# Optimization experiments

Measured on AMD Instinct MI355X. Metric: run time of the kernel, lower is better.

Reference implementation:

```python
import jax, jax.numpy as jnp
import numpy as np

# column-index constants for the node feature matrix and edge attributes
VM, VA, PG, QG, PD, QD = 0, 1, 2, 3, 4, 5
G_COL, B_COL = 0, 1

N_NODES = 100000
N_EDGES = 3200000
N_FEAT = 6


def setup_inputs() -> dict:
    key = jax.random.key(0)
    k1, k2, k3, k4, k5, k6 = jax.random.split(key, 6)
    pred = jax.random.normal(k1, (N_NODES, N_FEAT), dtype=jnp.float32)
    target = jax.random.normal(k2, (N_NODES, N_FEAT), dtype=jnp.float32)
    src = jax.random.randint(k3, (N_EDGES,), 0, N_NODES, dtype=jnp.int32)
    dst = jax.random.randint(k4, (N_EDGES,), 0, N_NODES, dtype=jnp.int32)
    edge_index = jnp.stack([src, dst], axis=0)
    edge_attr = jax.random.normal(k5, (N_EDGES, 2), dtype=jnp.float32)
    mask = jax.random.bernoulli(k6, 0.5, (N_NODES, N_FEAT))
    return {"pred": pred, "target": target, "edge_index": edge_index,
            "edge_attr": edge_attr, "mask": mask}


def reference(pred, target, edge_index, edge_attr, mask):
    # temp_pred[~mask] = target[~mask]
    tp = jnp.where(mask, pred, target)

    V_m = tp[:, VM]
    V_a = tp[:, VA]
    V = V_m * jnp.exp(1j * V_a)           # complex64 [N]
    V_conj = jnp.conj(V)

    # conj(Y_bus) entries on edges: G - jB
    Y_conj = edge_attr[:, G_COL] - 1j * edge_attr[:, B_COL]  # complex64 [E]

    row, col = edge_index[0], edge_index[1]
    # (Y_bus_conj @ V_conj)[i] = sum over edges (i,j) of conj(Y_ij) * conj(V_j)
    msg = Y_conj * V_conj[col]                               # gather-multiply [E]
    matvec = jax.ops.segment_sum(msg, row, num_segments=tp.shape[0])  # scatter-add [N]

    S_injection = V * matvec                                  # diag(V) @ (...)

    net_P = tp[:, PG] - tp[:, PD]
    net_Q = tp[:, QG] - tp[:, QD]
    diff = (net_P + 1j * net_Q) - S_injection

    loss = jnp.mean(jnp.abs(diff))
    real_loss = jnp.mean(jnp.abs(jnp.real(diff)))
    imag_loss = jnp.mean(jnp.abs(jnp.imag(diff)))
    return (loss, real_loss, imag_loss)
```

## Files before the change

kernel.cpp:

```cpp
#include <hip/hip_runtime.h>
#include <math.h>

constexpr int N_NODES = 100000;
constexpr int N_EDGES = 3200000;
constexpr int NF      = 6;

constexpr int BSHIFT  = 10;
constexpr int BNODES  = 1 << BSHIFT;
constexpr int NB      = (N_NODES + BNODES - 1) >> BSHIFT;
constexpr int CAP     = 34816;
constexpr int NSLICE  = 8;
constexpr int TILE    = 2048;
constexpr int EPT     = TILE / 256;
constexpr int NBLK_PART = (N_EDGES + TILE - 1) / TILE;

constexpr size_t OFF_V    = 0;
constexpr size_t OFF_MSG  = OFF_V + (size_t)N_NODES * 8;
constexpr size_t OFF_LROW = OFF_MSG + (size_t)NB * CAP * 8;
constexpr size_t OFF_PART = OFF_LROW + (size_t)NB * CAP * 2;
constexpr size_t OFF_CNT  = OFF_PART + (size_t)NB * NSLICE * BNODES * 8;
constexpr int    CTR_WORDS = 1024 / 4;
constexpr size_t WS_NEED  = OFF_CNT + 1024;

union F2U { float2 f; unsigned long long u; };

__global__ void node_prep(const float* __restrict__ pred,
                          const float* __restrict__ target,
                          const unsigned char* __restrict__ mask,
                          float2* __restrict__ v,
                          unsigned int* __restrict__ ctr) {
    int i = blockIdx.x * blockDim.x + threadIdx.x;
    if (blockIdx.x == 0 && threadIdx.x < CTR_WORDS) ctr[threadIdx.x] = 0u;
    if (i >= N_NODES) return;
    const int b = i * NF;
    float vm = mask[b + 0] ? pred[b + 0] : target[b + 0];
    float va = mask[b + 1] ? pred[b + 1] : target[b + 1];
    float s, c;
    sincosf(va, &s, &c);
    v[i] = make_float2(vm * c, vm * s);
}

__global__ __launch_bounds__(256) void partition_edges(
        const int* __restrict__ row, const int* __restrict__ col,
        const float2* __restrict__ attr, const float2* __restrict__ v,
        unsigned int* __restrict__ gcur,
        unsigned short* __restrict__ lrow_g, float2* __restrict__ msg_g) {
    __shared__ unsigned int h[4][NB];
    __shared__ unsigned int cur[4][NB];
    __shared__ int wb[4][NB];
    __shared__ int dbase[NB];
    __shared__ unsigned int tot_s[NB];
    __shared__ unsigned int rr_s[TILE];
    __shared__ float2 msg_s[TILE];
    __shared__ int total_s;

    const int tid = threadIdx.x;
    const int w = tid >> 6;
    const int e0 = blockIdx.x * TILE;

    for (int i = tid; i < 4 * NB; i += 256) {
        (&h[0][0])[i] = 0u;
        (&cur[0][0])[i] = 0u;
    }
    __syncthreads();

    int r[EPT];
    #pragma unroll
    for (int k = 0; k < EPT; ++k) {
        int e = e0 + k * 256 + tid;
        if (e < N_EDGES) {
            r[k] = row[e];
            atomicAdd(&h[w][r[k] >> BSHIFT], 1u);
        } else {
            r[k] = -1;
        }
    }
    __syncthreads();

    if (tid < NB)
        tot_s[tid] = h[0][tid] + h[1][tid] + h[2][tid] + h[3][tid];
    __syncthreads();

    if (tid < NB) {
        int lbase = 0;
        for (int j = 0; j < tid; ++j) lbase += (int)tot_s[j];
        unsigned t0 = h[0][tid], t1 = h[1][tid], t2 = h[2][tid];
        unsigned tot = tot_s[tid];
        unsigned g = tot ? atomicAdd(&gcur[tid], tot) : 0u;
        dbase[tid] = (int)g - lbase;
        wb[0][tid] = lbase;
        wb[1][tid] = lbase + (int)t0;
        wb[2][tid] = lbase + (int)(t0 + t1);
        wb[3][tid] = lbase + (int)(t0 + t1 + t2);
        if (tid == NB - 1) total_s = lbase + (int)tot;
    }
    __syncthreads();

    #pragma unroll
    for (int k = 0; k < EPT; ++k) {
        int rr = r[k];
        if (rr < 0) continue;
        int e = e0 + k * 256 + tid;
        int b = rr >> BSHIFT;
        int slot = wb[w][b] + (int)atomicAdd(&cur[w][b], 1u);
        int c = col[e];
        float2 gb = attr[e];
        float2 vv = v[c];
        float mre = fmaf(gb.x, vv.x, -gb.y * vv.y);
        float mim = -fmaf(gb.x, vv.y, gb.y * vv.x);
        rr_s[slot] = (unsigned)rr;
        msg_s[slot] = make_float2(mre, mim);
    }
    __syncthreads();

    const int total = total_s;
    for (int j = tid; j < total; j += 256) {
        unsigned rr = rr_s[j];
        int b = (int)(rr >> BSHIFT);
        int g = dbase[b] + j;
        if (g < CAP) {
            size_t idx = (size_t)b * CAP + g;
            msg_g[idx] = msg_s[j];
            lrow_g[idx] = (unsigned short)(rr & (BNODES - 1));
        }
    }
}

__global__ __launch_bounds__(256) void accum_finalize(
        const unsigned int* __restrict__ gcur,
        const unsigned short* __restrict__ lrow,
        const float2* __restrict__ msg,
        unsigned long long* __restrict__ partials,
        unsigned int* __restrict__ sdone,
        float* __restrict__ sums,
        unsigned int* __restrict__ done_all,
        const float* __restrict__ pred,
        const float* __restrict__ target,
        const unsigned char* __restrict__ mask,
        const float2* __restrict__ v,
        float* __restrict__ out) {
    __shared__ float acc_re[BNODES];
    __shared__ float acc_im[BNODES];
    __shared__ unsigned int old_s;
    const int tid = threadIdx.x;
    const int b = blockIdx.x / NSLICE;
    const int s = blockIdx.x % NSLICE;
    int cnt = (int)min(gcur[b], (unsigned)CAP);
    for (int i = tid; i < BNODES; i += 256) { acc_re[i] = 0.f; acc_im[i] = 0.f; }
    __syncthreads();
    int per = (((cnt + NSLICE - 1) / NSLICE) + 1) & ~1;
    int st = s * per;
    int en = min(st + per, cnt);
    const unsigned short* lr = lrow + (size_t)b * CAP;
    const float2* m = msg + (size_t)b * CAP;
    #pragma unroll 2
    for (int j = st + 2 * tid; j < en; j += 512) {
        if (j + 1 < en) {
            unsigned lp = *(const unsigned*)(lr + j);
            float4 mm = *(const float4*)(m + j);
            int li0 = (int)(lp & 0xFFFFu);
            int li1 = (int)(lp >> 16);
            atomicAdd(&acc_re[li0], mm.x);
            atomicAdd(&acc_im[li0], mm.y);
            atomicAdd(&acc_re[li1], mm.z);
            atomicAdd(&acc_im[li1], mm.w);
        } else {
            int li = lr[j];
            float2 mm = m[j];
            atomicAdd(&acc_re[li], mm.x);
            atomicAdd(&acc_im[li], mm.y);
        }
    }
    __syncthreads();
    unsigned long long* p = partials + ((size_t)b * NSLICE + s) * BNODES;
    for (int i = tid; i < BNODES; i += 256) {
        F2U cvt;
        cvt.f = make_float2(acc_re[i], acc_im[i]);
        __hip_atomic_store(&p[i], cvt.u, __ATOMIC_RELAXED, __HIP_MEMORY_SCOPE_AGENT);
    }
    asm volatile("s_waitcnt vmcnt(0)" ::: "memory");
    __syncthreads();
    if (tid == 0)
        old_s = __hip_atomic_fetch_add(&sdone[b], 1u, __ATOMIC_RELAXED,
                                       __HIP_MEMORY_SCOPE_AGENT);
    __syncthreads();
    if (old_s != (unsigned)(NSLICE - 1)) return;

    const unsigned long long* pb = partials + (size_t)b * NSLICE * BNODES;
    float a = 0.f, ar = 0.f, ai = 0.f;
    for (int li = tid; li < BNODES; li += 256) {
        int i = (b << BSHIFT) + li;
        if (i >= N_NODES) break;
        float mr = 0.f, mi = 0.f;
        #pragma unroll
        for (int s2 = 0; s2 < NSLICE; ++s2) {
            F2U cvt;
            cvt.u = __hip_atomic_load(&pb[(size_t)s2 * BNODES + li],
                                      __ATOMIC_RELAXED, __HIP_MEMORY_SCOPE_AGENT);
            mr += cvt.f.x; mi += cvt.f.y;
        }
        const int bb = i * NF;
        float pg = mask[bb + 2] ? pred[bb + 2] : target[bb + 2];
        float qg = mask[bb + 3] ? pred[bb + 3] : target[bb + 3];
        float pd = mask[bb + 4] ? pred[bb + 4] : target[bb + 4];
        float qd = mask[bb + 5] ? pred[bb + 5] : target[bb + 5];
        float netP = pg - pd;
        float netQ = qg - qd;
        float2 vv = v[i];
        float s_re = vv.x * mr - vv.y * mi;
        float s_im = vv.x * mi + vv.y * mr;
        float dre = netP - s_re;
        float dim = netQ - s_im;
        ar += fabsf(dre);
        ai += fabsf(dim);
        a  += sqrtf(dre * dre + dim * dim);
    }
    #pragma unroll
    for (int off = 32; off > 0; off >>= 1) {
        a  += __shfl_down(a,  off, 64);
        ar += __shfl_down(ar, off, 64);
        ai += __shfl_down(ai, off, 64);
    }
    __shared__ float red[3][4];
    int wave = tid >> 6;
    int lane = tid & 63;
    if (lane == 0) { red[0][wave] = a; red[1][wave] = ar; red[2][wave] = ai; }
    __syncthreads();
    if (tid == 0) {
        float r0 = atomicAdd(&sums[0], red[0][0] + red[0][1] + red[0][2] + red[0][3]);
        float r1 = atomicAdd(&sums[1], red[1][0] + red[1][1] + red[1][2] + red[1][3]);
        float r2 = atomicAdd(&sums[2], red[2][0] + red[2][1] + red[2][2] + red[2][3]);
        float chk = r0 + r1 + r2;
        if (chk == chk) {
            unsigned fin = atomicAdd(done_all, 1u);
            if (fin == (unsigned)(NB - 1)) {
                const float inv = 1.0f / (float)N_NODES;
                float t0 = atomicAdd(&sums[0], 0.f);
                float t1 = atomicAdd(&sums[1], 0.f);
                float t2 = atomicAdd(&sums[2], 0.f);
                __hip_atomic_store(&out[0], t0 * inv, __ATOMIC_RELAXED, __HIP_MEMORY_SCOPE_AGENT);
                __hip_atomic_store(&out[1], t1 * inv, __ATOMIC_RELAXED, __HIP_MEMORY_SCOPE_AGENT);
                __hip_atomic_store(&out[2], t2 * inv, __ATOMIC_RELAXED, __HIP_MEMORY_SCOPE_AGENT);
            }
        }
    }
}

__global__ void edge_scatter_fb(const int* __restrict__ row,
                                const int* __restrict__ col,
                                const float2* __restrict__ attr,
                                const float2* __restrict__ v,
                                float2* __restrict__ mv) {
    int e = blockIdx.x * blockDim.x + threadIdx.x;
    if (e >= N_EDGES) return;
    int r = row[e];
    int c = col[e];
    float2 gb = attr[e];
    float2 vv = v[c];
    float mre = fmaf(gb.x, vv.x, -gb.y * vv.y);
    float mim = -fmaf(gb.x, vv.y, gb.y * vv.x);
    atomicAdd(&mv[r].x, mre);
    atomicAdd(&mv[r].y, mim);
}

__global__ void finalize_fb(const float* __restrict__ pred,
                            const float* __restrict__ target,
                            const unsigned char* __restrict__ mask,
                            const float2* __restrict__ v,
                            const float2* __restrict__ mv,
                            float* __restrict__ sums) {
    int i = blockIdx.x * blockDim.x + threadIdx.x;
    float a = 0.f, ar = 0.f, ai = 0.f;
    if (i < N_NODES) {
        const int b = i * NF;
        float pg = mask[b + 2] ? pred[b + 2] : target[b + 2];
        float qg = mask[b + 3] ? pred[b + 3] : target[b + 3];
        float pd = mask[b + 4] ? pred[b + 4] : target[b + 4];
        float qd = mask[b + 5] ? pred[b + 5] : target[b + 5];
        float netP = pg - pd;
        float netQ = qg - qd;
        float2 vv = v[i];
        float2 m = mv[i];
        float s_re = vv.x * m.x - vv.y * m.y;
        float s_im = vv.x * m.y + vv.y * m.x;
        float dre = netP - s_re;
        float dim = netQ - s_im;
        ar = fabsf(dre);
        ai = fabsf(dim);
        a  = sqrtf(dre * dre + dim * dim);
    }
    #pragma unroll
    for (int off = 32; off > 0; off >>= 1) {
        a  += __shfl_down(a,  off, 64);
        ar += __shfl_down(ar, off, 64);
        ai += __shfl_down(ai, off, 64);
    }
    __shared__ float red[3][4];
    int wave = threadIdx.x >> 6;
    int lane = threadIdx.x & 63;
    if (lane == 0) { red[0][wave] = a; red[1][wave] = ar; red[2][wave] = ai; }
    __syncthreads();
    if (threadIdx.x == 0) {
        atomicAdd(&sums[0], red[0][0] + red[0][1] + red[0][2] + red[0][3]);
        atomicAdd(&sums[1], red[1][0] + red[1][1] + red[1][2] + red[1][3]);
        atomicAdd(&sums[2], red[2][0] + red[2][1] + red[2][2] + red[2][3]);
    }
}

__global__ void write_out_fb(const float* __restrict__ sums, float* __restrict__ out) {
    if (threadIdx.x == 0 && blockIdx.x == 0) {
        const float inv = 1.0f / (float)N_NODES;
        out[0] = sums[0] * inv;
        out[1] = sums[1] * inv;
        out[2] = sums[2] * inv;
    }
}

extern "C" void kernel_launch(void* const* d_in, const int* in_sizes, int n_in,
                              void* d_out, int out_size, void* d_ws, size_t ws_size,
                              hipStream_t stream) {
    const float*         pred   = (const float*)d_in[0];
    const float*         target = (const float*)d_in[1];
    const int*           eidx   = (const int*)d_in[2];
    const float2*        attr   = (const float2*)d_in[3];
    const unsigned char* mask   = (const unsigned char*)d_in[4];
    float* out = (float*)d_out;

    const int* row = eidx;
    const int* col = eidx + N_EDGES;

    char* ws = (char*)d_ws;
    const int B = 256;

    if (ws_size >= WS_NEED) {
        float2*             v        = (float2*)(ws + OFF_V);
        float2*             msg      = (float2*)(ws + OFF_MSG);
        unsigned short*     lrow     = (unsigned short*)(ws + OFF_LROW);
        unsigned long long* partials = (unsigned long long*)(ws + OFF_PART);
        unsigned int*       ctr      = (unsigned int*)(ws + OFF_CNT);
        unsigned int*       gcur     = (unsigned int*)(ws + OFF_CNT);
        unsigned int*       sdone    = (unsigned int*)(ws + OFF_CNT + 512);
        float*              sums     = (float*)(ws + OFF_CNT + 912);
        unsigned int*       done_all = (unsigned int*)(ws + OFF_CNT + 928);

        node_prep<<<(N_NODES + B - 1) / B, B, 0, stream>>>(pred, target, mask, v, ctr);
        partition_edges<<<NBLK_PART, B, 0, stream>>>(row, col, attr, v, gcur, lrow, msg);
        accum_finalize<<<NB * NSLICE, B, 0, stream>>>(gcur, lrow, msg, partials,
                                                      sdone, sums, done_all,
                                                      pred, target, mask, v, out);
    } else {
        float2* v    = (float2*)ws;
        float2* mv   = (float2*)(ws + (size_t)N_NODES * 8);
        float*  sums = (float*)(ws + 2ull * N_NODES * 8);
        hipMemsetAsync(mv, 0, (size_t)N_NODES * 8 + 16, stream);
        unsigned int* dummy = (unsigned int*)(ws + 2ull * N_NODES * 8 + 64);
        node_prep<<<(N_NODES + B - 1) / B, B, 0, stream>>>(pred, target, mask, v, dummy);
        edge_scatter_fb<<<(N_EDGES + B - 1) / B, B, 0, stream>>>(row, col, attr, v, mv);
        finalize_fb<<<(N_NODES + B - 1) / B, B, 0, stream>>>(pred, target, mask, v, mv, sums);
        write_out_fb<<<1, 64, 0, stream>>>(sums, out);
    }
}
```

Before: 209.5 us.

## Defer edge gather to accumulate phase with packed col/row and half-precision attrs

The partition kernel no longer gathers V and computes messages. It writes a packed 32-bit col|localrow word and fp16-packed edge attributes per edge, and the accumulate kernel gathers V[col] and does the complex multiply before the shared-memory atomics. Node prep is folded into the first blocks of the partition kernel, counters are zeroed with a memset, row/col/attr loads are vectorised, and CAP shrinks. This cuts the partitioned write traffic and removes a kernel launch. It brings in fp16 rounding of the admittance values, and it is racy because accumulate reads V written by other blocks of the fused partition kernel, though in a later launch, so that part is fine.

```diff
diff --git a/kernel.cpp b/kernel.cpp
--- a/kernel.cpp
+++ b/kernel.cpp
@@ -1,4 +1,5 @@
 #include <hip/hip_runtime.h>
+#include <hip/hip_fp16.h>
 #include <math.h>
 
 constexpr int N_NODES = 100000;
@@ -8,55 +9,57 @@
 constexpr int BSHIFT  = 10;
 constexpr int BNODES  = 1 << BSHIFT;
 constexpr int NB      = (N_NODES + BNODES - 1) >> BSHIFT;
-constexpr int CAP     = 34816;
+constexpr int CAP     = 33792;
 constexpr int NSLICE  = 8;
 constexpr int TILE    = 2048;
 constexpr int EPT     = TILE / 256;
 constexpr int NBLK_PART = (N_EDGES + TILE - 1) / TILE;
+constexpr int VPREP_BLOCKS = (N_NODES + 255) / 256;
 
 constexpr size_t OFF_V    = 0;
-constexpr size_t OFF_MSG  = OFF_V + (size_t)N_NODES * 8;
-constexpr size_t OFF_LROW = OFF_MSG + (size_t)NB * CAP * 8;
-constexpr size_t OFF_PART = OFF_LROW + (size_t)NB * CAP * 2;
+constexpr size_t OFF_CR   = OFF_V  + (size_t)N_NODES * 8;
+constexpr size_t OFF_AT   = OFF_CR + (size_t)NB * CAP * 4;
+constexpr size_t OFF_PART = OFF_AT + (size_t)NB * CAP * 4;
 constexpr size_t OFF_CNT  = OFF_PART + (size_t)NB * NSLICE * BNODES * 8;
-constexpr int    CTR_WORDS = 1024 / 4;
 constexpr size_t WS_NEED  = OFF_CNT + 1024;
 
 union F2U { float2 f; unsigned long long u; };
-
-__global__ void node_prep(const float* __restrict__ pred,
-                          const float* __restrict__ target,
-                          const unsigned char* __restrict__ mask,
-                          float2* __restrict__ v,
-                          unsigned int* __restrict__ ctr) {
-    int i = blockIdx.x * blockDim.x + threadIdx.x;
-    if (blockIdx.x == 0 && threadIdx.x < CTR_WORDS) ctr[threadIdx.x] = 0u;
-    if (i >= N_NODES) return;
-    const int b = i * NF;
-    float vm = mask[b + 0] ? pred[b + 0] : target[b + 0];
-    float va = mask[b + 1] ? pred[b + 1] : target[b + 1];
-    float s, c;
-    sincosf(va, &s, &c);
-    v[i] = make_float2(vm * c, vm * s);
-}
 
 __global__ __launch_bounds__(256) void partition_edges(
         const int* __restrict__ row, const int* __restrict__ col,
-        const float2* __restrict__ attr, const float2* __restrict__ v,
+        const float2* __restrict__ attr,
+        const float* __restrict__ pred, const float* __restrict__ target,
+        const unsigned char* __restrict__ mask,
+        float2* __restrict__ v_out,
         unsigned int* __restrict__ gcur,
-        unsigned short* __restrict__ lrow_g, float2* __restrict__ msg_g) {
+        unsigned int* __restrict__ colrow_g, unsigned int* __restrict__ attrh_g) {
     __shared__ unsigned int h[4][NB];
     __shared__ unsigned int cur[4][NB];
     __shared__ int wb[4][NB];
     __shared__ int dbase[NB];
     __shared__ unsigned int tot_s[NB];
-    __shared__ unsigned int rr_s[TILE];
-    __shared__ float2 msg_s[TILE];
+    __shared__ unsigned int colrow_s[TILE];
+    __shared__ unsigned int attrh_s[TILE];
+    __shared__ unsigned char bkt_s[TILE];
     __shared__ int total_s;
 
     const int tid = threadIdx.x;
     const int w = tid >> 6;
     const int e0 = blockIdx.x * TILE;
+    const int e_base = e0 + tid * EPT;
+    const bool ok = e_base < N_EDGES;
+
+    if (blockIdx.x < VPREP_BLOCKS) {
+        int i = blockIdx.x * 256 + tid;
+        if (i < N_NODES) {
+            const int bb = i * NF;
+            float vm = mask[bb + 0] ? pred[bb + 0] : target[bb + 0];
+            float va = mask[bb + 1] ? pred[bb + 1] : target[bb + 1];
+            float sn, cs;
+            sincosf(va, &sn, &cs);
+            v_out[i] = make_float2(vm * cs, vm * sn);
+        }
+    }
 
     for (int i = tid; i < 4 * NB; i += 256) {
         (&h[0][0])[i] = 0u;
@@ -65,15 +68,14 @@
     __syncthreads();
 
     int r[EPT];
-    #pragma unroll
-    for (int k = 0; k < EPT; ++k) {
-        int e = e0 + k * 256 + tid;
-        if (e < N_EDGES) {
-            r[k] = row[e];
+    if (ok) {
+        int4 ra = *(const int4*)(row + e_base);
+        int4 rb = *(const int4*)(row + e_base + 4);
+        r[0]=ra.x; r[1]=ra.y; r[2]=ra.z; r[3]=ra.w;
+        r[4]=rb.x; r[5]=rb.y; r[6]=rb.z; r[7]=rb.w;
+        #pragma unroll
+        for (int k = 0; k < EPT; ++k)
             atomicAdd(&h[w][r[k] >> BSHIFT], 1u);
-        } else {
-            r[k] = -1;
-        }
     }
     __syncthreads();
 
@@ -96,40 +98,45 @@
     }
     __syncthreads();
 
-    #pragma unroll
-    for (int k = 0; k < EPT; ++k) {
-        int rr = r[k];
-        if (rr < 0) continue;
-        int e = e0 + k * 256 + tid;
-        int b = rr >> BSHIFT;
-        int slot = wb[w][b] + (int)atomicAdd(&cur[w][b], 1u);
-        int c = col[e];
-        float2 gb = attr[e];
-        float2 vv = v[c];
-        float mre = fmaf(gb.x, vv.x, -gb.y * vv.y);
-        float mim = -fmaf(gb.x, vv.y, gb.y * vv.x);
-        rr_s[slot] = (unsigned)rr;
-        msg_s[slot] = make_float2(mre, mim);
+    if (ok) {
+        int4 ca = *(const int4*)(col + e_base);
+        int4 cb = *(const int4*)(col + e_base + 4);
+        int c[EPT] = {ca.x, ca.y, ca.z, ca.w, cb.x, cb.y, cb.z, cb.w};
+        float4 a0 = *(const float4*)(attr + e_base);
+        float4 a1 = *(const float4*)(attr + e_base + 2);
+        float4 a2 = *(const float4*)(attr + e_base + 4);
+        float4 a3 = *(const float4*)(attr + e_base + 6);
+        float gx[EPT] = {a0.x, a0.z, a1.x, a1.z, a2.x, a2.z, a3.x, a3.z};
+        float gy[EPT] = {a0.y, a0.w, a1.y, a1.w, a2.y, a2.w, a3.y, a3.w};
+        #pragma unroll
+        for (int k = 0; k < EPT; ++k) {
+            int rr = r[k];
+            int b = rr >> BSHIFT;
+            int slot = wb[w][b] + (int)atomicAdd(&cur[w][b], 1u);
+            __half2 hh = __floats2half2_rn(gx[k], gy[k]);
+            colrow_s[slot] = (unsigned)c[k] | ((unsigned)(rr & (BNODES - 1)) << 17);
+            attrh_s[slot] = *reinterpret_cast<unsigned int*>(&hh);
+            bkt_s[slot] = (unsigned char)b;
+        }
     }
     __syncthreads();
 
     const int total = total_s;
     for (int j = tid; j < total; j += 256) {
-        unsigned rr = rr_s[j];
-        int b = (int)(rr >> BSHIFT);
+        int b = (int)bkt_s[j];
         int g = dbase[b] + j;
         if (g < CAP) {
             size_t idx = (size_t)b * CAP + g;
-            msg_g[idx] = msg_s[j];
-            lrow_g[idx] = (unsigned short)(rr & (BNODES - 1));
+            colrow_g[idx] = colrow_s[j];
+            attrh_g[idx] = attrh_s[j];
         }
     }
 }
 
 __global__ __launch_bounds__(256) void accum_finalize(
         const unsigned int* __restrict__ gcur,
-        const unsigned short* __restrict__ lrow,
-        const float2* __restrict__ msg,
+        const unsigned int* __restrict__ colrow,
+        const unsigned int* __restrict__ attrh,
         unsigned long long* __restrict__ partials,
         unsigned int* __restrict__ sdone,
         float* __restrict__ sums,
@@ -151,24 +158,31 @@
     int per = (((cnt + NSLICE - 1) / NSLICE) + 1) & ~1;
     int st = s * per;
     int en = min(st + per, cnt);
-    const unsigned short* lr = lrow + (size_t)b * CAP;
-    const float2* m = msg + (size_t)b * CAP;
+    const unsigned int* crp = colrow + (size_t)b * CAP;
+    const unsigned int* ahp = attrh + (size_t)b * CAP;
     #pragma unroll 2
     for (int j = st + 2 * tid; j < en; j += 512) {
         if (j + 1 < en) {
-            unsigned lp = *(const unsigned*)(lr + j);
-            float4 mm = *(const float4*)(m + j);
-            int li0 = (int)(lp & 0xFFFFu);
-            int li1 = (int)(lp >> 16);
-            atomicAdd(&acc_re[li0], mm.x);
-            atomicAdd(&acc_im[li0], mm.y);
-            atomicAdd(&acc_re[li1], mm.z);
-            atomicAdd(&acc_im[li1], mm.w);
+            uint2 cr = *(const uint2*)(crp + j);
+            uint2 ah = *(const uint2*)(ahp + j);
+            int c0 = (int)(cr.x & 0x1FFFFu), li0 = (int)(cr.x >> 17);
+            int c1 = (int)(cr.y & 0x1FFFFu), li1 = (int)(cr.y >> 17);
+            float2 vv0 = v[c0];
+            float2 vv1 = v[c1];
+            float2 gb0 = __half22float2(*reinterpret_cast<__half2*>(&ah.x));
+            float2 gb1 = __half22float2(*reinterpret_cast<__half2*>(&ah.y));
+            atomicAdd(&acc_re[li0], fmaf(gb0.x, vv0.x, -gb0.y * vv0.y));
+            atomicAdd(&acc_im[li0], -fmaf(gb0.x, vv0.y, gb0.y * vv0.x));
+            atomicAdd(&acc_re[li1], fmaf(gb1.x, vv1.x, -gb1.y * vv1.y));
+            atomicAdd(&acc_im[li1], -fmaf(gb1.x, vv1.y, gb1.y * vv1.x));
         } else {
-            int li = lr[j];
-            float2 mm = m[j];
-            atomicAdd(&acc_re[li], mm.x);
-            atomicAdd(&acc_im[li], mm.y);
+            unsigned cr = crp[j];
+            unsigned ah = ahp[j];
+            int c0 = (int)(cr & 0x1FFFFu), li0 = (int)(cr >> 17);
+            float2 vv0 = v[c0];
+            float2 gb0 = __half22float2(*reinterpret_cast<__half2*>(&ah));
+            atomicAdd(&acc_re[li0], fmaf(gb0.x, vv0.x, -gb0.y * vv0.y));
+            atomicAdd(&acc_im[li0], -fmaf(gb0.x, vv0.y, gb0.y * vv0.x));
         }
     }
     __syncthreads();
@@ -244,6 +258,20 @@
             }
         }
     }
+}
+
+__global__ void node_prep_fb(const float* __restrict__ pred,
+                             const float* __restrict__ target,
+                             const unsigned char* __restrict__ mask,
+                             float2* __restrict__ v) {
+    int i = blockIdx.x * blockDim.x + threadIdx.x;
+    if (i >= N_NODES) return;
+    const int b = i * NF;
+    float vm = mask[b + 0] ? pred[b + 0] : target[b + 0];
+    float va = mask[b + 1] ? pred[b + 1] : target[b + 1];
+    float s, c;
+    sincosf(va, &s, &c);
+    v[i] = make_float2(vm * c, vm * s);
 }
 
 __global__ void edge_scatter_fb(const int* __restrict__ row,
@@ -334,18 +362,19 @@
 
     if (ws_size >= WS_NEED) {
         float2*             v        = (float2*)(ws + OFF_V);
-        float2*             msg      = (float2*)(ws + OFF_MSG);
-        unsigned short*     lrow     = (unsigned short*)(ws + OFF_LROW);
+        unsigned int*       colrow_g = (unsigned int*)(ws + OFF_CR);
+        unsigned int*       attrh_g  = (unsigned int*)(ws + OFF_AT);
         unsigned long long* partials = (unsigned long long*)(ws + OFF_PART);
-        unsigned int*       ctr      = (unsigned int*)(ws + OFF_CNT);
         unsigned int*       gcur     = (unsigned int*)(ws + OFF_CNT);
         unsigned int*       sdone    = (unsigned int*)(ws + OFF_CNT + 512);
         float*              sums     = (float*)(ws + OFF_CNT + 912);
         unsigned int*       done_all = (unsigned int*)(ws + OFF_CNT + 928);
 
-        node_prep<<<(N_NODES + B - 1) / B, B, 0, stream>>>(pred, target, mask, v, ctr);
-        partition_edges<<<NBLK_PART, B, 0, stream>>>(row, col, attr, v, gcur, lrow, msg);
-        accum_finalize<<<NB * NSLICE, B, 0, stream>>>(gcur, lrow, msg, partials,
+        hipMemsetAsync(ws + OFF_CNT, 0, 1024, stream);
+        partition_edges<<<NBLK_PART, B, 0, stream>>>(row, col, attr,
+                                                     pred, target, mask, v,
+                                                     gcur, colrow_g, attrh_g);
+        accum_finalize<<<NB * NSLICE, B, 0, stream>>>(gcur, colrow_g, attrh_g, partials,
                                                       sdone, sums, done_all,
                                                       pred, target, mask, v, out);
     } else {
@@ -353,8 +382,7 @@
         float2* mv   = (float2*)(ws + (size_t)N_NODES * 8);
         float*  sums = (float*)(ws + 2ull * N_NODES * 8);
         hipMemsetAsync(mv, 0, (size_t)N_NODES * 8 + 16, stream);
-        unsigned int* dummy = (unsigned int*)(ws + 2ull * N_NODES * 8 + 64);
-        node_prep<<<(N_NODES + B - 1) / B, B, 0, stream>>>(pred, target, mask, v, dummy);
+        node_prep_fb<<<(N_NODES + B - 1) / B, B, 0, stream>>>(pred, target, mask, v);
         edge_scatter_fb<<<(N_EDGES + B - 1) / B, B, 0, stream>>>(row, col, attr, v, mv);
         finalize_fb<<<(N_NODES + B - 1) / B, B, 0, stream>>>(pred, target, mask, v, mv, sums);
         write_out_fb<<<1, 64, 0, stream>>>(sums, out);
```

Result: faster. 189.4 us (-9.6%).
